# Performance work log

Measured on AMD Instinct MI355X. Metric: run time of the kernel, lower is better.

## Reference

```python
import jax, jax.numpy as jnp
import numpy as np

NEG_SLOPE = 0.2
STRONG_CONVEXITY = 0.5


def _scalar(x, Wq, Wl, bl, Wz, wz_out, wq_out, wl_out):
    # x: [B, D]; Wq/Wl: [L, H, D]; bl: [L, H]; Wz: [L-1, H, H]
    # Precompute all per-layer x-dependent terms in two batched einsums.
    qx = jnp.einsum('lhd,bd->lbh', Wq, x) ** 2          # [L, B, H]
    lx = jnp.einsum('lhd,bd->lbh', Wl, x) + bl[:, None, :]  # [L, B, H]
    z = jax.nn.leaky_relu(qx[0] + lx[0], negative_slope=NEG_SLOPE)

    def step(z, inputs):
        W, q, l = inputs
        z = jax.nn.leaky_relu(z @ W.T + q + l, negative_slope=NEG_SLOPE)
        return z, None

    z, _ = jax.lax.scan(step, z, (Wz, qx[1:], lx[1:]))
    # Final layer to scalar output (no bias on last wx_lin per torch code).
    out = z @ wz_out.T + (x @ wq_out.T) ** 2 + x @ wl_out.T  # [B, 1]
    return out


def setup_inputs() -> dict:
    key = jax.random.key(0)
    ks = jax.random.split(key, 8)
    B, D, H, L = 8192, 128, 512, 10
    f32 = jnp.float32
    x = jax.random.normal(ks[0], (B, D), f32)
    Wq = jax.random.normal(ks[1], (L, H, D), f32) * (1.0 / np.sqrt(D))
    Wl = jax.random.normal(ks[2], (L, H, D), f32) * (1.0 / np.sqrt(D))
    bl = jax.random.normal(ks[3], (L, H), f32) * 0.01
    # wz weights are kept non-negative in the original (clamp/exp init)
    Wz = jnp.abs(jax.random.normal(ks[4], (L - 1, H, H), f32)) * (1.0 / np.sqrt(H))
    wz_out = jnp.abs(jax.random.normal(ks[5], (1, H), f32)) * (1.0 / np.sqrt(H))
    wq_out = jax.random.normal(ks[6], (1, D), f32) * (1.0 / np.sqrt(D))
    wl_out = jax.random.normal(ks[7], (1, D), f32) * (1.0 / np.sqrt(D))
    return {"x": x, "Wq": Wq, "Wl": Wl, "bl": bl, "Wz": Wz,
            "wz_out": wz_out, "wq_out": wq_out, "wl_out": wl_out}


def reference(x, Wq, Wl, bl, Wz, wz_out, wq_out, wl_out):
    # forward = (1 - mu) * d(scalar)/dx + mu * x, with grad_outputs = ones
    def scalar_sum(xx):
        return jnp.sum(_scalar(xx, Wq, Wl, bl, Wz, wz_out, wq_out, wl_out))

    gx = jax.grad(scalar_sum)(x)  # per-sample gradient, [B, D]
    return (1.0 - STRONG_CONVEXITY) * gx + STRONG_CONVEXITY * x
```

## Files before the change

### kernel.cpp

```cpp
#include <hip/hip_runtime.h>


#define Bn 8192
#define Dn 128
#define Hn 512
#define Ln 10

constexpr float NS = 0.2f;

typedef __attribute__((ext_vector_type(8))) short short8;
typedef __attribute__((ext_vector_type(4))) float f32x4;

typedef const __attribute__((address_space(1))) void GV;
typedef __attribute__((address_space(3))) void LV;

__device__ __forceinline__ void gload16(const void* g, void* l) {
    __builtin_amdgcn_global_load_lds((GV*)g, (LV*)l, 16, 0, 0);
}

#define MFMA(acc, a, b) acc = __builtin_amdgcn_mfma_f32_16x16x32_bf16(a, b, acc, 0, 0, 0)

__device__ __forceinline__ unsigned short bf16_rne(float v) {
    unsigned u = __float_as_uint(v);
    u += 0x7FFFu + ((u >> 16) & 1u);
    return (unsigned short)(u >> 16);
}
__device__ __forceinline__ float bf2f(unsigned short h) {
    return __uint_as_float(((unsigned)h) << 16);
}
__device__ __forceinline__ void split2(float v, unsigned short& h, unsigned short& l) {
    h = bf16_rne(v);
    l = bf16_rne(v - bf2f(h));
}


__global__ __launch_bounds__(256) void split_flat(const float* __restrict__ in,
        unsigned short* __restrict__ hi, unsigned short* __restrict__ lo, int n4) {
    int i = blockIdx.x * 256 + threadIdx.x;
    if (i >= n4) return;
    float4 v = ((const float4*)in)[i];
    ushort4 h, l;
    split2(v.x, h.x, l.x);
    split2(v.y, h.y, l.y);
    split2(v.z, h.z, l.z);
    split2(v.w, h.w, l.w);
    ((ushort4*)hi)[i] = h;
    ((ushort4*)lo)[i] = l;
}

__global__ __launch_bounds__(256) void transpose_split(const float* __restrict__ in,
        unsigned short* __restrict__ hi, unsigned short* __restrict__ lo, int R, int C) {
    __shared__ float t[32][33];
    const size_t off = (size_t)blockIdx.z * R * C;
    const float* src = in + off;
    unsigned short* dh = hi + off;
    unsigned short* dl = lo + off;
    const int r0 = blockIdx.x * 32, c0 = blockIdx.y * 32;
    const int tr = threadIdx.x >> 5, tc = threadIdx.x & 31;
#pragma unroll
    for (int i = 0; i < 4; ++i)
        t[tr + 8 * i][tc] = src[(size_t)(r0 + tr + 8 * i) * C + c0 + tc];
    __syncthreads();
#pragma unroll
    for (int i = 0; i < 4; ++i) {
        float v = t[tc][tr + 8 * i];
        unsigned short h, l; split2(v, h, l);
        size_t o = (size_t)(c0 + tr + 8 * i) * R + r0 + tc;
        dh[o] = h; dl[o] = l;
    }
}


__global__ __launch_bounds__(256) void fwd_mfma(
    const unsigned short* __restrict__ xh, const unsigned short* __restrict__ xl,
    const unsigned short* __restrict__ zph, const unsigned short* __restrict__ zpl,
    const unsigned short* __restrict__ Wzh, const unsigned short* __restrict__ Wzl,
    const unsigned short* __restrict__ Wqh, const unsigned short* __restrict__ Wql,
    const unsigned short* __restrict__ Wlh, const unsigned short* __restrict__ Wll,
    const float* __restrict__ bl,
    unsigned short* __restrict__ zoh, unsigned short* __restrict__ zol,
    unsigned short* __restrict__ mask16, int hasZ)
{
    __shared__ __align__(16) char smem[32768];
    unsigned short* Ah  = (unsigned short*)smem;
    unsigned short* Al  = (unsigned short*)(smem + 8192);
    unsigned short* B0h = (unsigned short*)(smem + 16384);
    unsigned short* B0l = (unsigned short*)(smem + 20480);
    unsigned short* B1h = (unsigned short*)(smem + 24576);
    unsigned short* B1l = (unsigned short*)(smem + 28672);

    const int tid = threadIdx.x;
    const int w = tid >> 6, lane = tid & 63;
    const int lq = lane >> 4, lc = lane & 15;
    const int wm = (w & 1) * 64, wn = (w >> 1) * 32;
    const int row0 = blockIdx.x * 128, col0 = blockIdx.y * 64;
    const int sr = lane >> 2, sk = (lane & 3) * 8;

    f32x4 accz[4][2], accu[4][2], accv[4][2];
#pragma unroll
    for (int i = 0; i < 4; ++i)
#pragma unroll
        for (int j = 0; j < 2; ++j)
#pragma unroll
            for (int r = 0; r < 4; ++r) { accz[i][j][r] = 0.f; accu[i][j][r] = 0.f; accv[i][j][r] = 0.f; }

    if (hasZ) {
        for (int k0 = 0; k0 < Hn; k0 += 32) {
            __syncthreads();
            for (int c = w; c < 8; c += 4) {
                size_t go = (size_t)(row0 + c * 16 + sr) * Hn + k0 + sk;
                gload16(zph + go, Ah + c * 512);
                gload16(zpl + go, Al + c * 512);
            }
            {
                int c = w;
                size_t go = (size_t)(col0 + c * 16 + sr) * Hn + k0 + sk;
                gload16(Wzh + go, B0h + c * 512);
                gload16(Wzl + go, B0l + c * 512);
            }
            __syncthreads();
            short8 ah[4], al[4];
#pragma unroll
            for (int mt = 0; mt < 4; ++mt) {
                int ao = (wm + mt * 16 + lc) * 32 + lq * 8;
                ah[mt] = *(const short8*)(Ah + ao);
                al[mt] = *(const short8*)(Al + ao);
            }
#pragma unroll
            for (int nt = 0; nt < 2; ++nt) {
                int bo = (wn + nt * 16 + lc) * 32 + lq * 8;
                short8 bh = *(const short8*)(B0h + bo);
                short8 bv = *(const short8*)(B0l + bo);
#pragma unroll
                for (int mt = 0; mt < 4; ++mt) {
                    MFMA(accz[mt][nt], ah[mt], bh);
                    MFMA(accz[mt][nt], ah[mt], bv);
                    MFMA(accz[mt][nt], al[mt], bh);
                }
            }
        }
    }

    for (int k0 = 0; k0 < Dn; k0 += 32) {
        __syncthreads();
        for (int c = w; c < 8; c += 4) {
            size_t go = (size_t)(row0 + c * 16 + sr) * Dn + k0 + sk;
            gload16(xh + go, Ah + c * 512);
            gload16(xl + go, Al + c * 512);
        }
        {
            int c = w;
            size_t go = (size_t)(col0 + c * 16 + sr) * Dn + k0 + sk;
            gload16(Wqh + go, B0h + c * 512);
            gload16(Wql + go, B0l + c * 512);
            gload16(Wlh + go, B1h + c * 512);
            gload16(Wll + go, B1l + c * 512);
        }
        __syncthreads();
        short8 ah[4], al[4];
#pragma unroll
        for (int mt = 0; mt < 4; ++mt) {
            int ao = (wm + mt * 16 + lc) * 32 + lq * 8;
            ah[mt] = *(const short8*)(Ah + ao);
            al[mt] = *(const short8*)(Al + ao);
        }
#pragma unroll
        for (int nt = 0; nt < 2; ++nt) {
            int bo = (wn + nt * 16 + lc) * 32 + lq * 8;
            short8 bqh = *(const short8*)(B0h + bo);
            short8 bql = *(const short8*)(B0l + bo);
            short8 blh = *(const short8*)(B1h + bo);
            short8 bll = *(const short8*)(B1l + bo);
#pragma unroll
            for (int mt = 0; mt < 4; ++mt) {
                MFMA(accu[mt][nt], ah[mt], bqh);
                MFMA(accu[mt][nt], ah[mt], bql);
                MFMA(accu[mt][nt], al[mt], bqh);
                MFMA(accv[mt][nt], ah[mt], blh);
                MFMA(accv[mt][nt], ah[mt], bll);
                MFMA(accv[mt][nt], al[mt], blh);
            }
        }
    }

#pragma unroll
    for (int nt = 0; nt < 2; ++nt) {
        const int colb = col0 + wn + nt * 16;
        const int col = colb + lc;
        const float blv = bl[col];
#pragma unroll
        for (int mt = 0; mt < 4; ++mt) {
            const int rowb = row0 + wm + mt * 16;
#pragma unroll
            for (int r = 0; r < 4; ++r) {
                float uq = accu[mt][nt][r];
                float pre = accz[mt][nt][r] + uq * uq + accv[mt][nt][r] + blv;
                bool m = pre >= 0.f;
                unsigned long long bal = __ballot(m);
                if (lc == 0) {
                    int rw = rowb + lq * 4 + r;
                    mask16[(size_t)rw * 32 + (colb >> 4)] =
                        (unsigned short)((bal >> (lq * 16)) & 0xFFFFull);
                }
                float zv = m ? pre : NS * pre;
                unsigned short h, l; split2(zv, h, l);
                size_t o = (size_t)(rowb + lq * 4 + r) * Hn + col;
                zoh[o] = h; zol[o] = l;
            }
        }
    }
}


__global__ __launch_bounds__(256) void gemm_u_mfma(
    const unsigned short* __restrict__ xh, const unsigned short* __restrict__ xl,
    const unsigned short* __restrict__ Wqh, const unsigned short* __restrict__ Wql,
    float* __restrict__ u)
{
    __shared__ __align__(16) char smem[24576];
    unsigned short* Ah  = (unsigned short*)smem;
    unsigned short* Al  = (unsigned short*)(smem + 8192);
    unsigned short* B0h = (unsigned short*)(smem + 16384);
    unsigned short* B0l = (unsigned short*)(smem + 20480);

    const int tid = threadIdx.x;
    const int w = tid >> 6, lane = tid & 63;
    const int lq = lane >> 4, lc = lane & 15;
    const int wm = (w & 1) * 64, wn = (w >> 1) * 32;
    const int row0 = blockIdx.x * 128, col0 = blockIdx.y * 64;
    const int sr = lane >> 2, sk = (lane & 3) * 8;

    f32x4 acc[4][2];
#pragma unroll
    for (int i = 0; i < 4; ++i)
#pragma unroll
        for (int j = 0; j < 2; ++j)
#pragma unroll
            for (int r = 0; r < 4; ++r) acc[i][j][r] = 0.f;

    for (int k0 = 0; k0 < Dn; k0 += 32) {
        __syncthreads();
        for (int c = w; c < 8; c += 4) {
            size_t go = (size_t)(row0 + c * 16 + sr) * Dn + k0 + sk;
            gload16(xh + go, Ah + c * 512);
            gload16(xl + go, Al + c * 512);
        }
        {
            int c = w;
            size_t go = (size_t)(col0 + c * 16 + sr) * Dn + k0 + sk;
            gload16(Wqh + go, B0h + c * 512);
            gload16(Wql + go, B0l + c * 512);
        }
        __syncthreads();
        short8 ah[4], al[4];
#pragma unroll
        for (int mt = 0; mt < 4; ++mt) {
            int ao = (wm + mt * 16 + lc) * 32 + lq * 8;
            ah[mt] = *(const short8*)(Ah + ao);
            al[mt] = *(const short8*)(Al + ao);
        }
#pragma unroll
        for (int nt = 0; nt < 2; ++nt) {
            int bo = (wn + nt * 16 + lc) * 32 + lq * 8;
            short8 bh = *(const short8*)(B0h + bo);
            short8 bv = *(const short8*)(B0l + bo);
#pragma unroll
            for (int mt = 0; mt < 4; ++mt) {
                MFMA(acc[mt][nt], ah[mt], bh);
                MFMA(acc[mt][nt], ah[mt], bv);
                MFMA(acc[mt][nt], al[mt], bh);
            }
        }
    }

#pragma unroll
    for (int nt = 0; nt < 2; ++nt) {
        const int col = col0 + wn + nt * 16 + lc;
#pragma unroll
        for (int mt = 0; mt < 4; ++mt) {
            const int rowb = row0 + wm + mt * 16;
#pragma unroll
            for (int r = 0; r < 4; ++r)
                u[(size_t)(rowb + lq * 4 + r) * Hn + col] = acc[mt][nt][r];
        }
    }
}


__global__ __launch_bounds__(256) void bwd_g_mfma(
    const unsigned short* __restrict__ gah, const unsigned short* __restrict__ gal,
    const unsigned short* __restrict__ WzTh, const unsigned short* __restrict__ WzTl,
    const unsigned short* __restrict__ maskprev,
    unsigned short* __restrict__ goh, unsigned short* __restrict__ gol)
{
    __shared__ __align__(16) char smem[24576];
    unsigned short* Ah  = (unsigned short*)smem;
    unsigned short* Al  = (unsigned short*)(smem + 8192);
    unsigned short* B0h = (unsigned short*)(smem + 16384);
    unsigned short* B0l = (unsigned short*)(smem + 20480);

    const int tid = threadIdx.x;
    const int w = tid >> 6, lane = tid & 63;
    const int lq = lane >> 4, lc = lane & 15;
    const int wm = (w & 1) * 64, wn = (w >> 1) * 32;
    const int row0 = blockIdx.x * 128, col0 = blockIdx.y * 64;
    const int sr = lane >> 2, sk = (lane & 3) * 8;

    f32x4 acc[4][2];
#pragma unroll
    for (int i = 0; i < 4; ++i)
#pragma unroll
        for (int j = 0; j < 2; ++j)
#pragma unroll
            for (int r = 0; r < 4; ++r) acc[i][j][r] = 0.f;

    for (int k0 = 0; k0 < Hn; k0 += 32) {
        __syncthreads();
        for (int c = w; c < 8; c += 4) {
            size_t go = (size_t)(row0 + c * 16 + sr) * Hn + k0 + sk;
            gload16(gah + go, Ah + c * 512);
            gload16(gal + go, Al + c * 512);
        }
        {
            int c = w;
            size_t go = (size_t)(col0 + c * 16 + sr) * Hn + k0 + sk;
            gload16(WzTh + go, B0h + c * 512);
            gload16(WzTl + go, B0l + c * 512);
        }
        __syncthreads();
        short8 ah[4], al[4];
#pragma unroll
        for (int mt = 0; mt < 4; ++mt) {
            int ao = (wm + mt * 16 + lc) * 32 + lq * 8;
            ah[mt] = *(const short8*)(Ah + ao);
            al[mt] = *(const short8*)(Al + ao);
        }
#pragma unroll
        for (int nt = 0; nt < 2; ++nt) {
            int bo = (wn + nt * 16 + lc) * 32 + lq * 8;
            short8 bh = *(const short8*)(B0h + bo);
            short8 bv = *(const short8*)(B0l + bo);
#pragma unroll
            for (int mt = 0; mt < 4; ++mt) {
                MFMA(acc[mt][nt], ah[mt], bh);
                MFMA(acc[mt][nt], ah[mt], bv);
                MFMA(acc[mt][nt], al[mt], bh);
            }
        }
    }

#pragma unroll
    for (int nt = 0; nt < 2; ++nt) {
        const int colb = col0 + wn + nt * 16;
        const int col = colb + lc;
#pragma unroll
        for (int mt = 0; mt < 4; ++mt) {
            const int rowb = row0 + wm + mt * 16;
#pragma unroll
            for (int r = 0; r < 4; ++r) {
                int row = rowb + lq * 4 + r;
                unsigned short wbits = maskprev[(size_t)row * 32 + (colb >> 4)];
                float f = ((wbits >> lc) & 1) ? 1.f : NS;
                float v = acc[mt][nt][r] * f;
                unsigned short h, l; split2(v, h, l);
                size_t o = (size_t)row * Hn + col;
                goh[o] = h; gol[o] = l;
            }
        }
    }
}


__global__ __launch_bounds__(256) void bwd_x_mfma(
    const unsigned short* __restrict__ gah, const unsigned short* __restrict__ gal,
    const float* __restrict__ u,
    const unsigned short* __restrict__ WqTh, const unsigned short* __restrict__ WqTl,
    const unsigned short* __restrict__ WlTh, const unsigned short* __restrict__ WlTl,
    float* __restrict__ gx, int addTo)
{
    __shared__ __align__(16) char smem[32768];
    unsigned short* A1h = (unsigned short*)smem;
    unsigned short* A1l = (unsigned short*)(smem + 4096);
    unsigned short* A2h = (unsigned short*)(smem + 8192);
    unsigned short* A2l = (unsigned short*)(smem + 12288);
    unsigned short* Bqh = (unsigned short*)(smem + 16384);
    unsigned short* Bql = (unsigned short*)(smem + 20480);
    unsigned short* Blh = (unsigned short*)(smem + 24576);
    unsigned short* Bll = (unsigned short*)(smem + 28672);

    const int tid = threadIdx.x;
    const int w = tid >> 6, lane = tid & 63;
    const int lq = lane >> 4, lc = lane & 15;
    const int wm = (w & 1) * 32, wn = (w >> 1) * 32;
    const int row0 = blockIdx.x * 64, col0 = blockIdx.y * 64;
    const int sr = lane >> 2, sk = (lane & 3) * 8;
    const int ar = tid >> 2, as = (tid & 3) * 8;

    f32x4 acc[2][2];
#pragma unroll
    for (int i = 0; i < 2; ++i)
#pragma unroll
        for (int j = 0; j < 2; ++j)
#pragma unroll
            for (int r = 0; r < 4; ++r) acc[i][j][r] = 0.f;

    for (int k0 = 0; k0 < Hn; k0 += 32) {
        __syncthreads();
        {
            int c = w;
            size_t go = (size_t)(col0 + c * 16 + sr) * Hn + k0 + sk;
            gload16(WqTh + go, Bqh + c * 512);
            gload16(WqTl + go, Bql + c * 512);
            gload16(WlTh + go, Blh + c * 512);
            gload16(WlTl + go, Bll + c * 512);
        }
        {
            size_t gb = (size_t)(row0 + ar) * Hn + k0 + as;
            float4 u0 = *(const float4*)(u + gb);
            float4 u1 = *(const float4*)(u + gb + 4);
            ushort4 h0 = *(const ushort4*)(gah + gb);
            ushort4 h1 = *(const ushort4*)(gah + gb + 4);
            ushort4 l0 = *(const ushort4*)(gal + gb);
            ushort4 l1 = *(const ushort4*)(gal + gb + 4);
            int lo_ = ar * 32 + as;
            *(ushort4*)(A2h + lo_) = h0; *(ushort4*)(A2h + lo_ + 4) = h1;
            *(ushort4*)(A2l + lo_) = l0; *(ushort4*)(A2l + lo_ + 4) = l1;
            ushort4 oh, ol;
            float g, a1;
            g = bf2f(h0.x) + bf2f(l0.x); a1 = 2.f * u0.x * g; split2(a1, oh.x, ol.x);
            g = bf2f(h0.y) + bf2f(l0.y); a1 = 2.f * u0.y * g; split2(a1, oh.y, ol.y);
            g = bf2f(h0.z) + bf2f(l0.z); a1 = 2.f * u0.z * g; split2(a1, oh.z, ol.z);
            g = bf2f(h0.w) + bf2f(l0.w); a1 = 2.f * u0.w * g; split2(a1, oh.w, ol.w);
            *(ushort4*)(A1h + lo_) = oh; *(ushort4*)(A1l + lo_) = ol;
            g = bf2f(h1.x) + bf2f(l1.x); a1 = 2.f * u1.x * g; split2(a1, oh.x, ol.x);
            g = bf2f(h1.y) + bf2f(l1.y); a1 = 2.f * u1.y * g; split2(a1, oh.y, ol.y);
            g = bf2f(h1.z) + bf2f(l1.z); a1 = 2.f * u1.z * g; split2(a1, oh.z, ol.z);
            g = bf2f(h1.w) + bf2f(l1.w); a1 = 2.f * u1.w * g; split2(a1, oh.w, ol.w);
            *(ushort4*)(A1h + lo_ + 4) = oh; *(ushort4*)(A1l + lo_ + 4) = ol;
        }
        __syncthreads();
        short8 a1h[2], a1l[2], a2h[2], a2l[2];
#pragma unroll
        for (int mt = 0; mt < 2; ++mt) {
            int ao = (wm + mt * 16 + lc) * 32 + lq * 8;
            a1h[mt] = *(const short8*)(A1h + ao);
            a1l[mt] = *(const short8*)(A1l + ao);
            a2h[mt] = *(const short8*)(A2h + ao);
            a2l[mt] = *(const short8*)(A2l + ao);
        }
#pragma unroll
        for (int nt = 0; nt < 2; ++nt) {
            int bo = (wn + nt * 16 + lc) * 32 + lq * 8;
            short8 qh = *(const short8*)(Bqh + bo);
            short8 ql_ = *(const short8*)(Bql + bo);
            short8 lh = *(const short8*)(Blh + bo);
            short8 ll_ = *(const short8*)(Bll + bo);
#pragma unroll
            for (int mt = 0; mt < 2; ++mt) {
                MFMA(acc[mt][nt], a1h[mt], qh);
                MFMA(acc[mt][nt], a1h[mt], ql_);
                MFMA(acc[mt][nt], a1l[mt], qh);
                MFMA(acc[mt][nt], a2h[mt], lh);
                MFMA(acc[mt][nt], a2h[mt], ll_);
                MFMA(acc[mt][nt], a2l[mt], lh);
            }
        }
    }

#pragma unroll
    for (int nt = 0; nt < 2; ++nt) {
        const int col = col0 + wn + nt * 16 + lc;
#pragma unroll
        for (int mt = 0; mt < 2; ++mt) {
            const int rowb = row0 + wm + mt * 16;
#pragma unroll
            for (int r = 0; r < 4; ++r) {
                size_t o = (size_t)(rowb + lq * 4 + r) * Dn + col;
                float v = acc[mt][nt][r];
                if (addTo) v += gx[o];
                gx[o] = v;
            }
        }
    }
}


__global__ __launch_bounds__(256) void ga_init(
    const float* __restrict__ wz_out, const unsigned short* __restrict__ mask9,
    unsigned short* __restrict__ gh, unsigned short* __restrict__ gl)
{
    int i = blockIdx.x * 256 + threadIdx.x;
    int e = i << 2;
    int b = e >> 9, h = e & 511;
    unsigned short wbits = mask9[(size_t)b * 32 + (h >> 4)];
    float4 wv = *(const float4*)(wz_out + h);
    int sh = h & 15;
    ushort4 oh, ol;
    float f;
    f = wv.x * (((wbits >> (sh + 0)) & 1) ? 1.f : NS); split2(f, oh.x, ol.x);
    f = wv.y * (((wbits >> (sh + 1)) & 1) ? 1.f : NS); split2(f, oh.y, ol.y);
    f = wv.z * (((wbits >> (sh + 2)) & 1) ? 1.f : NS); split2(f, oh.z, ol.z);
    f = wv.w * (((wbits >> (sh + 3)) & 1) ? 1.f : NS); split2(f, oh.w, ol.w);
    *(ushort4*)(gh + e) = oh;
    *(ushort4*)(gl + e) = ol;
}

__global__ __launch_bounds__(256) void rowdot_kernel(
    const float* __restrict__ x, const float* __restrict__ wq_out, float* __restrict__ s) {
    const int b = blockIdx.x * 4 + (threadIdx.x >> 6);
    const int lane = threadIdx.x & 63;
    float v = x[(size_t)b * Dn + lane] * wq_out[lane] +
              x[(size_t)b * Dn + 64 + lane] * wq_out[64 + lane];
#pragma unroll
    for (int off = 32; off > 0; off >>= 1) v += __shfl_down(v, off, 64);
    if (lane == 0) s[b] = v;
}

__global__ __launch_bounds__(256) void final_kernel(
    float* __restrict__ out, const float* __restrict__ x, const float* __restrict__ s,
    const float* __restrict__ wq_out, const float* __restrict__ wl_out) {
    const int i = blockIdx.x * 256 + threadIdx.x;
    const int base = i << 2;
    const int b = base >> 7;
    const int d = base & (Dn - 1);
    float4 g = *(const float4*)(out + base);
    float4 xv = *(const float4*)(x + base);
    float4 wq = *(const float4*)(wq_out + d);
    float4 wl = *(const float4*)(wl_out + d);
    const float sb = s[b];
    float4 o;
    o.x = 0.5f * g.x + sb * wq.x + 0.5f * wl.x + 0.5f * xv.x;
    o.y = 0.5f * g.y + sb * wq.y + 0.5f * wl.y + 0.5f * xv.y;
    o.z = 0.5f * g.z + sb * wq.z + 0.5f * wl.z + 0.5f * xv.z;
    o.w = 0.5f * g.w + sb * wq.w + 0.5f * wl.w + 0.5f * xv.w;
    *(float4*)(out + base) = o;
}


extern "C" void kernel_launch(void* const* d_in, const int* in_sizes, int n_in,
                              void* d_out, int out_size, void* d_ws, size_t ws_size,
                              hipStream_t stream) {
    (void)in_sizes; (void)n_in; (void)out_size; (void)ws_size;
    const float* x      = (const float*)d_in[0];
    const float* Wq     = (const float*)d_in[1];
    const float* Wl     = (const float*)d_in[2];
    const float* bl     = (const float*)d_in[3];
    const float* Wz     = (const float*)d_in[4];
    const float* wz_out = (const float*)d_in[5];
    const float* wq_out = (const float*)d_in[6];
    const float* wl_out = (const float*)d_in[7];
    float* out = (float*)d_out;

    char* p = (char*)d_ws;
    #define CARVE(name, bytes) unsigned short* name = (unsigned short*)p; p += (((size_t)(bytes)) + 255) & ~(size_t)255;
    CARVE(xh,  (size_t)Bn*Dn*2)  CARVE(xl,  (size_t)Bn*Dn*2)
    CARVE(Wqh, (size_t)Ln*Hn*Dn*2) CARVE(Wql, (size_t)Ln*Hn*Dn*2)
    CARVE(Wlh, (size_t)Ln*Hn*Dn*2) CARVE(Wll, (size_t)Ln*Hn*Dn*2)
    CARVE(WqTh,(size_t)Ln*Hn*Dn*2) CARVE(WqTl,(size_t)Ln*Hn*Dn*2)
    CARVE(WlTh,(size_t)Ln*Hn*Dn*2) CARVE(WlTl,(size_t)Ln*Hn*Dn*2)
    CARVE(Wzh, (size_t)(Ln-1)*Hn*Hn*2) CARVE(Wzl, (size_t)(Ln-1)*Hn*Hn*2)
    CARVE(WzTh,(size_t)(Ln-1)*Hn*Hn*2) CARVE(WzTl,(size_t)(Ln-1)*Hn*Hn*2)
    CARVE(zAh, (size_t)Bn*Hn*2) CARVE(zAl, (size_t)Bn*Hn*2)
    CARVE(zBh, (size_t)Bn*Hn*2) CARVE(zBl, (size_t)Bn*Hn*2)
    float* uBuf = (float*)p; p += (size_t)Bn*Hn*4;
    float* s    = (float*)p; p += (size_t)Bn*4;
    unsigned short* mask16 = (unsigned short*)p; p += (size_t)Ln*Bn*32*2;
    #undef CARVE

    split_flat<<<(Bn*Dn/4 + 255)/256, 256, 0, stream>>>(x, xh, xl, Bn*Dn/4);
    split_flat<<<(Ln*Hn*Dn/4 + 255)/256, 256, 0, stream>>>(Wq, Wqh, Wql, Ln*Hn*Dn/4);
    split_flat<<<(Ln*Hn*Dn/4 + 255)/256, 256, 0, stream>>>(Wl, Wlh, Wll, Ln*Hn*Dn/4);
    split_flat<<<((Ln-1)*Hn*Hn/4 + 255)/256, 256, 0, stream>>>(Wz, Wzh, Wzl, (Ln-1)*Hn*Hn/4);
    transpose_split<<<dim3(Hn/32, Dn/32, Ln), 256, 0, stream>>>(Wq, WqTh, WqTl, Hn, Dn);
    transpose_split<<<dim3(Hn/32, Dn/32, Ln), 256, 0, stream>>>(Wl, WlTh, WlTl, Hn, Dn);
    transpose_split<<<dim3(Hn/32, Hn/32, Ln-1), 256, 0, stream>>>(Wz, WzTh, WzTl, Hn, Hn);

    rowdot_kernel<<<Bn/4, 256, 0, stream>>>(x, wq_out, s);

    const dim3 gF(Bn/128, Hn/64);

    fwd_mfma<<<gF, 256, 0, stream>>>(xh, xl, nullptr, nullptr, nullptr, nullptr,
        Wqh, Wql, Wlh, Wll, bl, zAh, zAl, mask16, 0);
    for (int l = 1; l < Ln; ++l) {
        const unsigned short* zh  = (l & 1) ? zAh : zBh;
        const unsigned short* zl_ = (l & 1) ? zAl : zBl;
        unsigned short* oh  = (l & 1) ? zBh : zAh;
        unsigned short* ol_ = (l & 1) ? zBl : zAl;
        fwd_mfma<<<gF, 256, 0, stream>>>(xh, xl, zh, zl_,
            Wzh + (size_t)(l-1)*Hn*Hn, Wzl + (size_t)(l-1)*Hn*Hn,
            Wqh + (size_t)l*Hn*Dn, Wql + (size_t)l*Hn*Dn,
            Wlh + (size_t)l*Hn*Dn, Wll + (size_t)l*Hn*Dn,
            bl + (size_t)l*Hn, oh, ol_, mask16 + (size_t)l*Bn*32, 1);
    }

    ga_init<<<(Bn*Hn/4)/256, 256, 0, stream>>>(wz_out, mask16 + (size_t)9*Bn*32, zAh, zAl);
    for (int l = Ln - 1; l >= 0; --l) {
        int sidx = (Ln - 1 - l) & 1;
        const unsigned short* gh_ = sidx ? zBh : zAh;
        const unsigned short* gl_ = sidx ? zBl : zAl;
        gemm_u_mfma<<<gF, 256, 0, stream>>>(xh, xl,
            Wqh + (size_t)l*Hn*Dn, Wql + (size_t)l*Hn*Dn, uBuf);
        bwd_x_mfma<<<dim3(Bn/64, Dn/64), 256, 0, stream>>>(gh_, gl_, uBuf,
            WqTh + (size_t)l*Dn*Hn, WqTl + (size_t)l*Dn*Hn,
            WlTh + (size_t)l*Dn*Hn, WlTl + (size_t)l*Dn*Hn,
            out, (l == Ln - 1) ? 0 : 1);
        if (l > 0) {
            unsigned short* oh  = sidx ? zAh : zBh;
            unsigned short* ol_ = sidx ? zAl : zBl;
            bwd_g_mfma<<<gF, 256, 0, stream>>>(gh_, gl_,
                WzTh + (size_t)(l-1)*Hn*Hn, WzTl + (size_t)(l-1)*Hn*Hn,
                mask16 + (size_t)(l-1)*Bn*32, oh, ol_);
        }
    }

    final_kernel<<<(Bn*Dn/4)/256, 256, 0, stream>>>(out, x, s, wq_out, wl_out);
}
```

Baseline: 930.9 us.

## Precompute all-layer Wq·x once and fuse backward g/x kernels per layer

```diff
diff --git a/kernel.cpp b/kernel.cpp
--- a/kernel.cpp
+++ b/kernel.cpp
@@ -5,6 +5,7 @@
 #define Dn 128
 #define Hn 512
 #define Ln 10
+#define NW (Ln * Hn)
 
 constexpr float NS = 0.2f;
 
@@ -71,23 +72,93 @@
 }
 
 
+__global__ __launch_bounds__(256) void gemm_uall(
+    const unsigned short* __restrict__ xh, const unsigned short* __restrict__ xl,
+    const unsigned short* __restrict__ Wh, const unsigned short* __restrict__ Wv,
+    float* __restrict__ u)
+{
+    __shared__ __align__(16) char smem[32768];
+    unsigned short* Ah = (unsigned short*)smem;
+    unsigned short* Al = (unsigned short*)(smem + 8192);
+    unsigned short* Bh = (unsigned short*)(smem + 16384);
+    unsigned short* Bl = (unsigned short*)(smem + 24576);
+
+    const int tid = threadIdx.x;
+    const int w = tid >> 6, lane = tid & 63;
+    const int lq = lane >> 4, lc = lane & 15;
+    const int wm = (w & 1) * 64, wn = (w >> 1) * 64;
+    const int row0 = blockIdx.x * 128, col0 = blockIdx.y * 128;
+    const int sr = lane >> 2, sk = (lane & 3) * 8;
+
+    f32x4 acc[4][4];
+#pragma unroll
+    for (int i = 0; i < 4; ++i)
+#pragma unroll
+        for (int j = 0; j < 4; ++j)
+#pragma unroll
+            for (int r = 0; r < 4; ++r) acc[i][j][r] = 0.f;
+
+    for (int k0 = 0; k0 < Dn; k0 += 32) {
+        __syncthreads();
+        for (int c = w; c < 8; c += 4) {
+            size_t ga_ = (size_t)(row0 + c * 16 + sr) * Dn + k0 + sk;
+            gload16(xh + ga_, Ah + c * 512);
+            gload16(xl + ga_, Al + c * 512);
+            size_t gb = (size_t)(col0 + c * 16 + sr) * Dn + k0 + sk;
+            gload16(Wh + gb, Bh + c * 512);
+            gload16(Wv + gb, Bl + c * 512);
+        }
+        __syncthreads();
+        short8 ah[4], al[4];
+#pragma unroll
+        for (int mt = 0; mt < 4; ++mt) {
+            int ao = (wm + mt * 16 + lc) * 32 + lq * 8;
+            ah[mt] = *(const short8*)(Ah + ao);
+            al[mt] = *(const short8*)(Al + ao);
+        }
+#pragma unroll
+        for (int nt = 0; nt < 4; ++nt) {
+            int bo = (wn + nt * 16 + lc) * 32 + lq * 8;
+            short8 bh = *(const short8*)(Bh + bo);
+            short8 bv = *(const short8*)(Bl + bo);
+#pragma unroll
+            for (int mt = 0; mt < 4; ++mt) {
+                MFMA(acc[mt][nt], ah[mt], bh);
+                MFMA(acc[mt][nt], ah[mt], bv);
+                MFMA(acc[mt][nt], al[mt], bh);
+            }
+        }
+    }
+
+#pragma unroll
+    for (int nt = 0; nt < 4; ++nt) {
+        const int col = col0 + wn + nt * 16 + lc;
+#pragma unroll
+        for (int mt = 0; mt < 4; ++mt) {
+            const int rowb = row0 + wm + mt * 16;
+#pragma unroll
+            for (int r = 0; r < 4; ++r)
+                u[(size_t)(rowb + lq * 4 + r) * NW + col] = acc[mt][nt][r];
+        }
+    }
+}
+
+
 __global__ __launch_bounds__(256) void fwd_mfma(
     const unsigned short* __restrict__ xh, const unsigned short* __restrict__ xl,
     const unsigned short* __restrict__ zph, const unsigned short* __restrict__ zpl,
     const unsigned short* __restrict__ Wzh, const unsigned short* __restrict__ Wzl,
-    const unsigned short* __restrict__ Wqh, const unsigned short* __restrict__ Wql,
     const unsigned short* __restrict__ Wlh, const unsigned short* __restrict__ Wll,
     const float* __restrict__ bl,
+    const float* __restrict__ u,
     unsigned short* __restrict__ zoh, unsigned short* __restrict__ zol,
     unsigned short* __restrict__ mask16, int hasZ)
 {
-    __shared__ __align__(16) char smem[32768];
-    unsigned short* Ah  = (unsigned short*)smem;
-    unsigned short* Al  = (unsigned short*)(smem + 8192);
-    unsigned short* B0h = (unsigned short*)(smem + 16384);
-    unsigned short* B0l = (unsigned short*)(smem + 20480);
-    unsigned short* B1h = (unsigned short*)(smem + 24576);
-    unsigned short* B1l = (unsigned short*)(smem + 28672);
+    __shared__ __align__(16) char smem[24576];
+    unsigned short* Ah = (unsigned short*)smem;
+    unsigned short* Al = (unsigned short*)(smem + 8192);
+    unsigned short* Bh = (unsigned short*)(smem + 16384);
+    unsigned short* Bl = (unsigned short*)(smem + 20480);
 
     const int tid = threadIdx.x;
     const int w = tid >> 6, lane = tid & 63;
@@ -96,13 +167,13 @@
     const int row0 = blockIdx.x * 128, col0 = blockIdx.y * 64;
     const int sr = lane >> 2, sk = (lane & 3) * 8;
 
-    f32x4 accz[4][2], accu[4][2], accv[4][2];
+    f32x4 acc[4][2];
 #pragma unroll
     for (int i = 0; i < 4; ++i)
 #pragma unroll
         for (int j = 0; j < 2; ++j)
 #pragma unroll
-            for (int r = 0; r < 4; ++r) { accz[i][j][r] = 0.f; accu[i][j][r] = 0.f; accv[i][j][r] = 0.f; }
+            for (int r = 0; r < 4; ++r) acc[i][j][r] = 0.f;
 
     if (hasZ) {
         for (int k0 = 0; k0 < Hn; k0 += 32) {
@@ -115,8 +186,8 @@
             {
                 int c = w;
                 size_t go = (size_t)(col0 + c * 16 + sr) * Hn + k0 + sk;
-                gload16(Wzh + go, B0h + c * 512);
-                gload16(Wzl + go, B0l + c * 512);
+                gload16(Wzh + go, Bh + c * 512);
+                gload16(Wzl + go, Bl + c * 512);
             }
             __syncthreads();
             short8 ah[4], al[4];
@@ -129,13 +200,13 @@
 #pragma unroll
             for (int nt = 0; nt < 2; ++nt) {
                 int bo = (wn + nt * 16 + lc) * 32 + lq * 8;
-                short8 bh = *(const short8*)(B0h + bo);
-                short8 bv = *(const short8*)(B0l + bo);
+                short8 bh = *(const short8*)(Bh + bo);
+                short8 bv = *(const short8*)(Bl + bo);
 #pragma unroll
                 for (int mt = 0; mt < 4; ++mt) {
-                    MFMA(accz[mt][nt], ah[mt], bh);
-                    MFMA(accz[mt][nt], ah[mt], bv);
-                    MFMA(accz[mt][nt], al[mt], bh);
+                    MFMA(acc[mt][nt], ah[mt], bh);
+                    MFMA(acc[mt][nt], ah[mt], bv);
+                    MFMA(acc[mt][nt], al[mt], bh);
                 }
             }
         }
@@ -151,10 +222,8 @@
         {
             int c = w;
             size_t go = (size_t)(col0 + c * 16 + sr) * Dn + k0 + sk;
-            gload16(Wqh + go, B0h + c * 512);
-            gload16(Wql + go, B0l + c * 512);
-            gload16(Wlh + go, B1h + c * 512);
-            gload16(Wll + go, B1l + c * 512);
+            gload16(Wlh + go, Bh + c * 512);
+            gload16(Wll + go, Bl + c * 512);
         }
         __syncthreads();
         short8 ah[4], al[4];
@@ -167,18 +236,13 @@
 #pragma unroll
         for (int nt = 0; nt < 2; ++nt) {
             int bo = (wn + nt * 16 + lc) * 32 + lq * 8;
-            short8 bqh = *(const short8*)(B0h + bo);
-            short8 bql = *(const short8*)(B0l + bo);
-            short8 blh = *(const short8*)(B1h + bo);
-            short8 bll = *(const short8*)(B1l + bo);
-#pragma unroll
-            for (int mt = 0; mt < 4; ++mt) {
-                MFMA(accu[mt][nt], ah[mt], bqh);
-                MFMA(accu[mt][nt], ah[mt], bql);
-                MFMA(accu[mt][nt], al[mt], bqh);
-                MFMA(accv[mt][nt], ah[mt], blh);
-                MFMA(accv[mt][nt], ah[mt], bll);
-                MFMA(accv[mt][nt], al[mt], blh);
+            short8 bh = *(const short8*)(Bh + bo);
+            short8 bv = *(const short8*)(Bl + bo);
+#pragma unroll
+            for (int mt = 0; mt < 4; ++mt) {
+                MFMA(acc[mt][nt], ah[mt], bh);
+                MFMA(acc[mt][nt], ah[mt], bv);
+                MFMA(acc[mt][nt], al[mt], bh);
             }
         }
     }
@@ -193,18 +257,18 @@
             const int rowb = row0 + wm + mt * 16;
 #pragma unroll
             for (int r = 0; r < 4; ++r) {
-                float uq = accu[mt][nt][r];
-                float pre = accz[mt][nt][r] + uq * uq + accv[mt][nt][r] + blv;
+                const int row = rowb + lq * 4 + r;
+                float uq = u[(size_t)row * NW + col];
+                float pre = acc[mt][nt][r] + uq * uq + blv;
                 bool m = pre >= 0.f;
                 unsigned long long bal = __ballot(m);
                 if (lc == 0) {
-                    int rw = rowb + lq * 4 + r;
-                    mask16[(size_t)rw * 32 + (colb >> 4)] =
+                    mask16[(size_t)row * 32 + (colb >> 4)] =
                         (unsigned short)((bal >> (lq * 16)) & 0xFFFFull);
                 }
                 float zv = m ? pre : NS * pre;
                 unsigned short h, l; split2(zv, h, l);
-                size_t o = (size_t)(rowb + lq * 4 + r) * Hn + col;
+                size_t o = (size_t)row * Hn + col;
                 zoh[o] = h; zol[o] = l;
             }
         }
@@ -212,22 +276,22 @@
 }
 
 
-__global__ __launch_bounds__(256) void gemm_u_mfma(
-    const unsigned short* __restrict__ xh, const unsigned short* __restrict__ xl,
-    const unsigned short* __restrict__ Wqh, const unsigned short* __restrict__ Wql,
-    float* __restrict__ u)
+__global__ __launch_bounds__(256) void bwd_mfma(
+    const unsigned short* __restrict__ gah, const unsigned short* __restrict__ gal,
+    const unsigned short* __restrict__ WzTh, const unsigned short* __restrict__ WzTl,
+    const unsigned short* __restrict__ maskprev,
+    unsigned short* __restrict__ goh, unsigned short* __restrict__ gol,
+    const float* __restrict__ u,
+    const unsigned short* __restrict__ WqTh, const unsigned short* __restrict__ WqTl,
+    const unsigned short* __restrict__ WlTh, const unsigned short* __restrict__ WlTl,
+    float* __restrict__ gx, int addTo, int nWz)
 {
-    __shared__ __align__(16) char smem[24576];
-    unsigned short* Ah  = (unsigned short*)smem;
-    unsigned short* Al  = (unsigned short*)(smem + 8192);
-    unsigned short* B0h = (unsigned short*)(smem + 16384);
-    unsigned short* B0l = (unsigned short*)(smem + 20480);
-
+    __shared__ __align__(16) char smem[49152];
     const int tid = threadIdx.x;
     const int w = tid >> 6, lane = tid & 63;
     const int lq = lane >> 4, lc = lane & 15;
     const int wm = (w & 1) * 64, wn = (w >> 1) * 32;
-    const int row0 = blockIdx.x * 128, col0 = blockIdx.y * 64;
+    const int row0 = blockIdx.x * 128;
     const int sr = lane >> 2, sk = (lane & 3) * 8;
 
     f32x4 acc[4][2];
@@ -238,247 +302,154 @@
 #pragma unroll
             for (int r = 0; r < 4; ++r) acc[i][j][r] = 0.f;
 
-    for (int k0 = 0; k0 < Dn; k0 += 32) {
-        __syncthreads();
-        for (int c = w; c < 8; c += 4) {
-            size_t go = (size_t)(row0 + c * 16 + sr) * Dn + k0 + sk;
-            gload16(xh + go, Ah + c * 512);
-            gload16(xl + go, Al + c * 512);
-        }
-        {
-            int c = w;
-            size_t go = (size_t)(col0 + c * 16 + sr) * Dn + k0 + sk;
-            gload16(Wqh + go, B0h + c * 512);
-            gload16(Wql + go, B0l + c * 512);
-        }
-        __syncthreads();
-        short8 ah[4], al[4];
-#pragma unroll
-        for (int mt = 0; mt < 4; ++mt) {
-            int ao = (wm + mt * 16 + lc) * 32 + lq * 8;
-            ah[mt] = *(const short8*)(Ah + ao);
-            al[mt] = *(const short8*)(Al + ao);
-        }
+    if ((int)blockIdx.y < nWz) {
+        const int col0 = blockIdx.y * 64;
+        unsigned short* Ah = (unsigned short*)smem;
+        unsigned short* Al = (unsigned short*)(smem + 8192);
+        unsigned short* Bh = (unsigned short*)(smem + 16384);
+        unsigned short* Bl = (unsigned short*)(smem + 20480);
+
+        for (int k0 = 0; k0 < Hn; k0 += 32) {
+            __syncthreads();
+            for (int c = w; c < 8; c += 4) {
+                size_t go = (size_t)(row0 + c * 16 + sr) * Hn + k0 + sk;
+                gload16(gah + go, Ah + c * 512);
+                gload16(gal + go, Al + c * 512);
+            }
+            {
+                int c = w;
+                size_t go = (size_t)(col0 + c * 16 + sr) * Hn + k0 + sk;
+                gload16(WzTh + go, Bh + c * 512);
+                gload16(WzTl + go, Bl + c * 512);
+            }
+            __syncthreads();
+            short8 ah[4], al[4];
+#pragma unroll
+            for (int mt = 0; mt < 4; ++mt) {
+                int ao = (wm + mt * 16 + lc) * 32 + lq * 8;
+                ah[mt] = *(const short8*)(Ah + ao);
+                al[mt] = *(const short8*)(Al + ao);
+            }
+#pragma unroll
+            for (int nt = 0; nt < 2; ++nt) {
+                int bo = (wn + nt * 16 + lc) * 32 + lq * 8;
+                short8 bh = *(const short8*)(Bh + bo);
+                short8 bv = *(const short8*)(Bl + bo);
+#pragma unroll
+                for (int mt = 0; mt < 4; ++mt) {
+                    MFMA(acc[mt][nt], ah[mt], bh);
+                    MFMA(acc[mt][nt], ah[mt], bv);
+                    MFMA(acc[mt][nt], al[mt], bh);
+                }
+            }
+        }
+
 #pragma unroll
         for (int nt = 0; nt < 2; ++nt) {
-            int bo = (wn + nt * 16 + lc) * 32 + lq * 8;
-            short8 bh = *(const short8*)(B0h + bo);
-            short8 bv = *(const short8*)(B0l + bo);
-#pragma unroll
-            for (int mt = 0; mt < 4; ++mt) {
-                MFMA(acc[mt][nt], ah[mt], bh);
-                MFMA(acc[mt][nt], ah[mt], bv);
-                MFMA(acc[mt][nt], al[mt], bh);
-            }
-        }
-    }
-
-#pragma unroll
-    for (int nt = 0; nt < 2; ++nt) {
-        const int col = col0 + wn + nt * 16 + lc;
-#pragma unroll
-        for (int mt = 0; mt < 4; ++mt) {
-            const int rowb = row0 + wm + mt * 16;
-#pragma unroll
-            for (int r = 0; r < 4; ++r)
-                u[(size_t)(rowb + lq * 4 + r) * Hn + col] = acc[mt][nt][r];
-        }
-    }
-}
-
-
-__global__ __launch_bounds__(256) void bwd_g_mfma(
-    const unsigned short* __restrict__ gah, const unsigned short* __restrict__ gal,
-    const unsigned short* __restrict__ WzTh, const unsigned short* __restrict__ WzTl,
-    const unsigned short* __restrict__ maskprev,
-    unsigned short* __restrict__ goh, unsigned short* __restrict__ gol)
-{
-    __shared__ __align__(16) char smem[24576];
-    unsigned short* Ah  = (unsigned short*)smem;
-    unsigned short* Al  = (unsigned short*)(smem + 8192);
-    unsigned short* B0h = (unsigned short*)(smem + 16384);
-    unsigned short* B0l = (unsigned short*)(smem + 20480);
-
-    const int tid = threadIdx.x;
-    const int w = tid >> 6, lane = tid & 63;
-    const int lq = lane >> 4, lc = lane & 15;
-    const int wm = (w & 1) * 64, wn = (w >> 1) * 32;
-    const int row0 = blockIdx.x * 128, col0 = blockIdx.y * 64;
-    const int sr = lane >> 2, sk = (lane & 3) * 8;
-
-    f32x4 acc[4][2];
-#pragma unroll
-    for (int i = 0; i < 4; ++i)
-#pragma unroll
-        for (int j = 0; j < 2; ++j)
-#pragma unroll
-            for (int r = 0; r < 4; ++r) acc[i][j][r] = 0.f;
-
-    for (int k0 = 0; k0 < Hn; k0 += 32) {
-        __syncthreads();
-        for (int c = w; c < 8; c += 4) {
-            size_t go = (size_t)(row0 + c * 16 + sr) * Hn + k0 + sk;
-            gload16(gah + go, Ah + c * 512);
-            gload16(gal + go, Al + c * 512);
-        }
-        {
-            int c = w;
-            size_t go = (size_t)(col0 + c * 16 + sr) * Hn + k0 + sk;
-            gload16(WzTh + go, B0h + c * 512);
-            gload16(WzTl + go, B0l + c * 512);
-        }
-        __syncthreads();
-        short8 ah[4], al[4];
-#pragma unroll
-        for (int mt = 0; mt < 4; ++mt) {
-            int ao = (wm + mt * 16 + lc) * 32 + lq * 8;
-            ah[mt] = *(const short8*)(Ah + ao);
-            al[mt] = *(const short8*)(Al + ao);
-        }
+            const int colb = col0 + wn + nt * 16;
+            const int col = colb + lc;
+#pragma unroll
+            for (int mt = 0; mt < 4; ++mt) {
+                const int rowb = row0 + wm + mt * 16;
+#pragma unroll
+                for (int r = 0; r < 4; ++r) {
+                    int row = rowb + lq * 4 + r;
+                    unsigned short wbits = maskprev[(size_t)row * 32 + (colb >> 4)];
+                    float f = ((wbits >> lc) & 1) ? 1.f : NS;
+                    float v = acc[mt][nt][r] * f;
+                    unsigned short h, l; split2(v, h, l);
+                    size_t o = (size_t)row * Hn + col;
+                    goh[o] = h; gol[o] = l;
+                }
+            }
+        }
+    } else {
+        const int col0 = ((int)blockIdx.y - nWz) * 64;
+        unsigned short* A1h = (unsigned short*)smem;
+        unsigned short* A1l = (unsigned short*)(smem + 8192);
+        unsigned short* A2h = (unsigned short*)(smem + 16384);
+        unsigned short* A2l = (unsigned short*)(smem + 24576);
+        unsigned short* Bqh = (unsigned short*)(smem + 32768);
+        unsigned short* Bql = (unsigned short*)(smem + 36864);
+        unsigned short* Blh = (unsigned short*)(smem + 40960);
+        unsigned short* Bll = (unsigned short*)(smem + 45056);
+
+        const int ar = tid >> 1;
+        const int as = (tid & 1) * 16;
+
+        for (int k0 = 0; k0 < Hn; k0 += 32) {
+            __syncthreads();
+            {
+                int c = w;
+                size_t go = (size_t)(col0 + c * 16 + sr) * Hn + k0 + sk;
+                gload16(WqTh + go, Bqh + c * 512);
+                gload16(WqTl + go, Bql + c * 512);
+                gload16(WlTh + go, Blh + c * 512);
+                gload16(WlTl + go, Bll + c * 512);
+            }
+            {
+                size_t gb = (size_t)(row0 + ar) * Hn + k0 + as;
+                const float* urow = u + (size_t)(row0 + ar) * NW + k0 + as;
+                int lo_ = ar * 32 + as;
+#pragma unroll
+                for (int t4 = 0; t4 < 4; ++t4) {
+                    float4 uv = *(const float4*)(urow + t4 * 4);
+                    ushort4 h = *(const ushort4*)(gah + gb + t4 * 4);
+                    ushort4 lw = *(const ushort4*)(gal + gb + t4 * 4);
+                    *(ushort4*)(A2h + lo_ + t4 * 4) = h;
+                    *(ushort4*)(A2l + lo_ + t4 * 4) = lw;
+                    ushort4 oh, ol;
+                    float g, a1;
+                    g = bf2f(h.x) + bf2f(lw.x); a1 = 2.f * uv.x * g; split2(a1, oh.x, ol.x);
+                    g = bf2f(h.y) + bf2f(lw.y); a1 = 2.f * uv.y * g; split2(a1, oh.y, ol.y);
+                    g = bf2f(h.z) + bf2f(lw.z); a1 = 2.f * uv.z * g; split2(a1, oh.z, ol.z);
+                    g = bf2f(h.w) + bf2f(lw.w); a1 = 2.f * uv.w * g; split2(a1, oh.w, ol.w);
+                    *(ushort4*)(A1h + lo_ + t4 * 4) = oh;
+                    *(ushort4*)(A1l + lo_ + t4 * 4) = ol;
+                }
+            }
+            __syncthreads();
+            short8 a1h[4], a1l[4], a2h[4], a2l[4];
+#pragma unroll
+            for (int mt = 0; mt < 4; ++mt) {
+                int ao = (wm + mt * 16 + lc) * 32 + lq * 8;
+                a1h[mt] = *(const short8*)(A1h + ao);
+                a1l[mt] = *(const short8*)(A1l + ao);
+                a2h[mt] = *(const short8*)(A2h + ao);
+                a2l[mt] = *(const short8*)(A2l + ao);
+            }
+#pragma unroll
+            for (int nt = 0; nt < 2; ++nt) {
+                int bo = (wn + nt * 16 + lc) * 32 + lq * 8;
+                short8 qh = *(const short8*)(Bqh + bo);
+                short8 ql_ = *(const short8*)(Bql + bo);
+                short8 lh = *(const short8*)(Blh + bo);
+                short8 ll_ = *(const short8*)(Bll + bo);
+#pragma unroll
+                for (int mt = 0; mt < 4; ++mt) {
+                    MFMA(acc[mt][nt], a1h[mt], qh);
+                    MFMA(acc[mt][nt], a1h[mt], ql_);
+                    MFMA(acc[mt][nt], a1l[mt], qh);
+                    MFMA(acc[mt][nt], a2h[mt], lh);
+                    MFMA(acc[mt][nt], a2h[mt], ll_);
+                    MFMA(acc[mt][nt], a2l[mt], lh);
+                }
+            }
+        }
+
 #pragma unroll
         for (int nt = 0; nt < 2; ++nt) {
-            int bo = (wn + nt * 16 + lc) * 32 + lq * 8;
-            short8 bh = *(const short8*)(B0h + bo);
-            short8 bv = *(const short8*)(B0l + bo);
-#pragma unroll
-            for (int mt = 0; mt < 4; ++mt) {
-                MFMA(acc[mt][nt], ah[mt], bh);
-                MFMA(acc[mt][nt], ah[mt], bv);
-                MFMA(acc[mt][nt], al[mt], bh);
-            }
-        }
-    }
-
-#pragma unroll
-    for (int nt = 0; nt < 2; ++nt) {
-        const int colb = col0 + wn + nt * 16;
-        const int col = colb + lc;
-#pragma unroll
-        for (int mt = 0; mt < 4; ++mt) {
-            const int rowb = row0 + wm + mt * 16;
-#pragma unroll
-            for (int r = 0; r < 4; ++r) {
-                int row = rowb + lq * 4 + r;
-                unsigned short wbits = maskprev[(size_t)row * 32 + (colb >> 4)];
-                float f = ((wbits >> lc) & 1) ? 1.f : NS;
-                float v = acc[mt][nt][r] * f;
-                unsigned short h, l; split2(v, h, l);
-                size_t o = (size_t)row * Hn + col;
-                goh[o] = h; gol[o] = l;
-            }
-        }
-    }
-}
-
-
-__global__ __launch_bounds__(256) void bwd_x_mfma(
-    const unsigned short* __restrict__ gah, const unsigned short* __restrict__ gal,
-    const float* __restrict__ u,
-    const unsigned short* __restrict__ WqTh, const unsigned short* __restrict__ WqTl,
-    const unsigned short* __restrict__ WlTh, const unsigned short* __restrict__ WlTl,
-    float* __restrict__ gx, int addTo)
-{
-    __shared__ __align__(16) char smem[32768];
-    unsigned short* A1h = (unsigned short*)smem;
-    unsigned short* A1l = (unsigned short*)(smem + 4096);
-    unsigned short* A2h = (unsigned short*)(smem + 8192);
-    unsigned short* A2l = (unsigned short*)(smem + 12288);
-    unsigned short* Bqh = (unsigned short*)(smem + 16384);
-    unsigned short* Bql = (unsigned short*)(smem + 20480);
-    unsigned short* Blh = (unsigned short*)(smem + 24576);
-    unsigned short* Bll = (unsigned short*)(smem + 28672);
-
-    const int tid = threadIdx.x;
-    const int w = tid >> 6, lane = tid & 63;
-    const int lq = lane >> 4, lc = lane & 15;
-    const int wm = (w & 1) * 32, wn = (w >> 1) * 32;
-    const int row0 = blockIdx.x * 64, col0 = blockIdx.y * 64;
-    const int sr = lane >> 2, sk = (lane & 3) * 8;
-    const int ar = tid >> 2, as = (tid & 3) * 8;
-
-    f32x4 acc[2][2];
-#pragma unroll
-    for (int i = 0; i < 2; ++i)
-#pragma unroll
-        for (int j = 0; j < 2; ++j)
-#pragma unroll
-            for (int r = 0; r < 4; ++r) acc[i][j][r] = 0.f;
-
-    for (int k0 = 0; k0 < Hn; k0 += 32) {
-        __syncthreads();
-        {
-            int c = w;
-            size_t go = (size_t)(col0 + c * 16 + sr) * Hn + k0 + sk;
-            gload16(WqTh + go, Bqh + c * 512);
-            gload16(WqTl + go, Bql + c * 512);
-            gload16(WlTh + go, Blh + c * 512);
-            gload16(WlTl + go, Bll + c * 512);
-        }
-        {
-            size_t gb = (size_t)(row0 + ar) * Hn + k0 + as;
-            float4 u0 = *(const float4*)(u + gb);
-            float4 u1 = *(const float4*)(u + gb + 4);
-            ushort4 h0 = *(const ushort4*)(gah + gb);
-            ushort4 h1 = *(const ushort4*)(gah + gb + 4);
-            ushort4 l0 = *(const ushort4*)(gal + gb);
-            ushort4 l1 = *(const ushort4*)(gal + gb + 4);
-            int lo_ = ar * 32 + as;
-            *(ushort4*)(A2h + lo_) = h0; *(ushort4*)(A2h + lo_ + 4) = h1;
-            *(ushort4*)(A2l + lo_) = l0; *(ushort4*)(A2l + lo_ + 4) = l1;
-            ushort4 oh, ol;
-            float g, a1;
-            g = bf2f(h0.x) + bf2f(l0.x); a1 = 2.f * u0.x * g; split2(a1, oh.x, ol.x);
-            g = bf2f(h0.y) + bf2f(l0.y); a1 = 2.f * u0.y * g; split2(a1, oh.y, ol.y);
-            g = bf2f(h0.z) + bf2f(l0.z); a1 = 2.f * u0.z * g; split2(a1, oh.z, ol.z);
-            g = bf2f(h0.w) + bf2f(l0.w); a1 = 2.f * u0.w * g; split2(a1, oh.w, ol.w);
-            *(ushort4*)(A1h + lo_) = oh; *(ushort4*)(A1l + lo_) = ol;
-            g = bf2f(h1.x) + bf2f(l1.x); a1 = 2.f * u1.x * g; split2(a1, oh.x, ol.x);
-            g = bf2f(h1.y) + bf2f(l1.y); a1 = 2.f * u1.y * g; split2(a1, oh.y, ol.y);
-            g = bf2f(h1.z) + bf2f(l1.z); a1 = 2.f * u1.z * g; split2(a1, oh.z, ol.z);
-            g = bf2f(h1.w) + bf2f(l1.w); a1 = 2.f * u1.w * g; split2(a1, oh.w, ol.w);
-            *(ushort4*)(A1h + lo_ + 4) = oh; *(ushort4*)(A1l + lo_ + 4) = ol;
-        }
-        __syncthreads();
-        short8 a1h[2], a1l[2], a2h[2], a2l[2];
-#pragma unroll
-        for (int mt = 0; mt < 2; ++mt) {
-            int ao = (wm + mt * 16 + lc) * 32 + lq * 8;
-            a1h[mt] = *(const short8*)(A1h + ao);
-            a1l[mt] = *(const short8*)(A1l + ao);
-            a2h[mt] = *(const short8*)(A2h + ao);
-            a2l[mt] = *(const short8*)(A2l + ao);
-        }
-#pragma unroll
-        for (int nt = 0; nt < 2; ++nt) {
-            int bo = (wn + nt * 16 + lc) * 32 + lq * 8;
-            short8 qh = *(const short8*)(Bqh + bo);
-            short8 ql_ = *(const short8*)(Bql + bo);
-            short8 lh = *(const short8*)(Blh + bo);
-            short8 ll_ = *(const short8*)(Bll + bo);
-#pragma unroll
-            for (int mt = 0; mt < 2; ++mt) {
-                MFMA(acc[mt][nt], a1h[mt], qh);
-                MFMA(acc[mt][nt], a1h[mt], ql_);
-                MFMA(acc[mt][nt], a1l[mt], qh);
-                MFMA(acc[mt][nt], a2h[mt], lh);
-                MFMA(acc[mt][nt], a2h[mt], ll_);
-                MFMA(acc[mt][nt], a2l[mt], lh);
-            }
-        }
-    }
-
-#pragma unroll
-    for (int nt = 0; nt < 2; ++nt) {
-        const int col = col0 + wn + nt * 16 + lc;
-#pragma unroll
-        for (int mt = 0; mt < 2; ++mt) {
-            const int rowb = row0 + wm + mt * 16;
-#pragma unroll
-            for (int r = 0; r < 4; ++r) {
-                size_t o = (size_t)(rowb + lq * 4 + r) * Dn + col;
-                float v = acc[mt][nt][r];
-                if (addTo) v += gx[o];
-                gx[o] = v;
+            const int col = col0 + wn + nt * 16 + lc;
+#pragma unroll
+            for (int mt = 0; mt < 4; ++mt) {
+                const int rowb = row0 + wm + mt * 16;
+#pragma unroll
+                for (int r = 0; r < 4; ++r) {
+                    size_t o = (size_t)(rowb + lq * 4 + r) * Dn + col;
+                    float v = acc[mt][nt][r];
+                    if (addTo) v += gx[o];
+                    gx[o] = v;
+                }
             }
         }
     }
@@ -562,9 +533,9 @@
     CARVE(WzTh,(size_t)(Ln-1)*Hn*Hn*2) CARVE(WzTl,(size_t)(Ln-1)*Hn*Hn*2)
     CARVE(zAh, (size_t)Bn*Hn*2) CARVE(zAl, (size_t)Bn*Hn*2)
     CARVE(zBh, (size_t)Bn*Hn*2) CARVE(zBl, (size_t)Bn*Hn*2)
-    float* uBuf = (float*)p; p += (size_t)Bn*Hn*4;
-    float* s    = (float*)p; p += (size_t)Bn*4;
-    unsigned short* mask16 = (unsigned short*)p; p += (size_t)Ln*Bn*32*2;
+    CARVE(mask16, (size_t)Ln*Bn*32*2)
+    float* s = (float*)p; p += (size_t)Bn*4 + 256;
+    float* uall = (float*)p; p += (size_t)Bn*NW*4;
     #undef CARVE
 
     split_flat<<<(Bn*Dn/4 + 255)/256, 256, 0, stream>>>(x, xh, xl, Bn*Dn/4);
@@ -577,10 +548,12 @@
 
     rowdot_kernel<<<Bn/4, 256, 0, stream>>>(x, wq_out, s);
 
+    gemm_uall<<<dim3(Bn/128, NW/128), 256, 0, stream>>>(xh, xl, Wqh, Wql, uall);
+
     const dim3 gF(Bn/128, Hn/64);
 
     fwd_mfma<<<gF, 256, 0, stream>>>(xh, xl, nullptr, nullptr, nullptr, nullptr,
-        Wqh, Wql, Wlh, Wll, bl, zAh, zAl, mask16, 0);
+        Wlh, Wll, bl, uall, zAh, zAl, mask16, 0);
     for (int l = 1; l < Ln; ++l) {
         const unsigned short* zh  = (l & 1) ? zAh : zBh;
         const unsigned short* zl_ = (l & 1) ? zAl : zBl;
@@ -588,9 +561,9 @@
         unsigned short* ol_ = (l & 1) ? zBl : zAl;
         fwd_mfma<<<gF, 256, 0, stream>>>(xh, xl, zh, zl_,
             Wzh + (size_t)(l-1)*Hn*Hn, Wzl + (size_t)(l-1)*Hn*Hn,
-            Wqh + (size_t)l*Hn*Dn, Wql + (size_t)l*Hn*Dn,
             Wlh + (size_t)l*Hn*Dn, Wll + (size_t)l*Hn*Dn,
-            bl + (size_t)l*Hn, oh, ol_, mask16 + (size_t)l*Bn*32, 1);
+            bl + (size_t)l*Hn, uall + (size_t)l*Hn,
+            oh, ol_, mask16 + (size_t)l*Bn*32, 1);
     }
 
     ga_init<<<(Bn*Hn/4)/256, 256, 0, stream>>>(wz_out, mask16 + (size_t)9*Bn*32, zAh, zAl);
@@ -598,19 +571,19 @@
         int sidx = (Ln - 1 - l) & 1;
         const unsigned short* gh_ = sidx ? zBh : zAh;
         const unsigned short* gl_ = sidx ? zBl : zAl;
-        gemm_u_mfma<<<gF, 256, 0, stream>>>(xh, xl,
-            Wqh + (size_t)l*Hn*Dn, Wql + (size_t)l*Hn*Dn, uBuf);
-        bwd_x_mfma<<<dim3(Bn/64, Dn/64), 256, 0, stream>>>(gh_, gl_, uBuf,
+        unsigned short* oh  = sidx ? zAh : zBh;
+        unsigned short* ol_ = sidx ? zAl : zBl;
+        const int nWz = (l > 0) ? 8 : 0;
+        bwd_mfma<<<dim3(Bn/128, nWz + 2), 256, 0, stream>>>(
+            gh_, gl_,
+            (l > 0) ? WzTh + (size_t)(l-1)*Hn*Hn : WzTh,
+            (l > 0) ? WzTl + (size_t)(l-1)*Hn*Hn : WzTl,
+            (l > 0) ? mask16 + (size_t)(l-1)*Bn*32 : mask16,
+            oh, ol_,
+            uall + (size_t)l*Hn,
             WqTh + (size_t)l*Dn*Hn, WqTl + (size_t)l*Dn*Hn,
             WlTh + (size_t)l*Dn*Hn, WlTl + (size_t)l*Dn*Hn,
-            out, (l == Ln - 1) ? 0 : 1);
-        if (l > 0) {
-            unsigned short* oh  = sidx ? zAh : zBh;
-            unsigned short* ol_ = sidx ? zAl : zBl;
-            bwd_g_mfma<<<gF, 256, 0, stream>>>(gh_, gl_,
-                WzTh + (size_t)(l-1)*Hn*Hn, WzTl + (size_t)(l-1)*Hn*Hn,
-                mask16 + (size_t)(l-1)*Bn*32, oh, ol_);
-        }
+            out, (l == Ln - 1) ? 0 : 1, nWz);
     }
 
     final_kernel<<<(Bn*Dn/4)/256, 256, 0, stream>>>(out, x, s, wq_out, wl_out);
```

After: 1.026 ms. +10.3%, slower.
